# Optimization experiments

Measured on AMD Instinct MI355X. Metric: run time of the kernel, lower is better.

The kernel has to match this reference:

```python
import jax, jax.numpy as jnp
import numpy as np

N, E, HDIM, EDIM, MSG_H, UPD_H = 50000, 640000, 128, 32, 128, 128
LN_EPS = 1e-5


def setup_inputs() -> dict:
    key = jax.random.key(0)
    ks = jax.random.split(key, 12)
    def lin(k, fan_in, fan_out):
        return jax.random.normal(k, (fan_in, fan_out), dtype=jnp.float32) / np.sqrt(fan_in)
    h = jax.random.normal(ks[0], (N, HDIM), dtype=jnp.float32)
    edge_index = jax.random.randint(ks[1], (2, E), 0, N, dtype=jnp.int32)
    edge_attr = jax.random.normal(ks[2], (E, EDIM), dtype=jnp.float32)
    return {
        "h": h,
        "edge_index": edge_index,
        "edge_attr": edge_attr,
        # edge MLP: Linear(2*hdim+edim -> msg_hidden), ReLU, Linear(msg_hidden -> hdim)
        "ew1": lin(ks[3], 2 * HDIM + EDIM, MSG_H),
        "eb1": jnp.zeros((MSG_H,), jnp.float32),
        "ew2": lin(ks[4], MSG_H, HDIM),
        "eb2": jnp.zeros((HDIM,), jnp.float32),
        # node MLP: Linear(2*hdim -> upd_hidden), ReLU, Linear(upd_hidden -> hdim)
        "nw1": lin(ks[5], 2 * HDIM, UPD_H),
        "nb1": jnp.zeros((UPD_H,), jnp.float32),
        "nw2": lin(ks[6], UPD_H, HDIM),
        "nb2": jnp.zeros((HDIM,), jnp.float32),
        # LayerNorm(hdim)
        "gamma": jnp.ones((HDIM,), jnp.float32),
        "beta": jnp.zeros((HDIM,), jnp.float32),
    }


def reference(h, edge_index, edge_attr, ew1, eb1, ew2, eb2, nw1, nb1, nw2, nb2, gamma, beta):
    src, dst = edge_index[0], edge_index[1]
    # gather + concat -> edge MLP  (eval mode: dropout inactive, edge_dropout off)
    m_in = jnp.concatenate([h[src], h[dst], edge_attr], axis=1)       # [E, 2H+EDIM]
    m = jax.nn.relu(m_in @ ew1 + eb1) @ ew2 + eb2                     # [E, H]
    # scatter-add messages into destination nodes
    agg = jax.ops.segment_sum(m, dst, num_segments=h.shape[0])        # [N, H]
    # node update MLP
    u_in = jnp.concatenate([h, agg], axis=1)                          # [N, 2H]
    h_upd = jax.nn.relu(u_in @ nw1 + nb1) @ nw2 + nb2                 # [N, H]
    # residual + LayerNorm
    x = h + h_upd
    mu = jnp.mean(x, axis=-1, keepdims=True)
    var = jnp.mean(jnp.square(x - mu), axis=-1, keepdims=True)
    return (x - mu) * jax.lax.rsqrt(var + LN_EPS) * gamma + beta
```

## Files before the change

### kernel.cpp

```cpp
#include <hip/hip_runtime.h>
#include <cstdint>

#define HD 128
#define ED 32
#define BME 64
#define BMN 128
#define PAD_E 296
#define PAD_N 264
#define PAD_T 136
#define EGRID 512

typedef _Float16 f16;
typedef __attribute__((ext_vector_type(2))) _Float16 f16x2;
typedef __attribute__((ext_vector_type(4))) _Float16 f16x4;
typedef __attribute__((ext_vector_type(8))) _Float16 f16x8;
typedef __attribute__((ext_vector_type(4))) float    f32x4;

__device__ __forceinline__ f32x4 mfma16(f16x8 a, f16x8 b, f32x4 c) {
    return __builtin_amdgcn_mfma_f32_16x16x32_f16(a, b, c, 0, 0, 0);
}
__device__ __forceinline__ f16x8 cvt8(const float* p) {
    const float4 a0 = *(const float4*)p;
    const float4 a1 = *(const float4*)(p + 4);
    f16x8 v;
    v[0] = (f16)a0.x; v[1] = (f16)a0.y; v[2] = (f16)a0.z; v[3] = (f16)a0.w;
    v[4] = (f16)a1.x; v[5] = (f16)a1.y; v[6] = (f16)a1.z; v[7] = (f16)a1.w;
    return v;
}

__global__ __launch_bounds__(256) void zero_f32(float4* p, long n4) {
    long i = (long)blockIdx.x * blockDim.x + threadIdx.x;
    const long stride = (long)gridDim.x * blockDim.x;
    const float4 z = make_float4(0.f, 0.f, 0.f, 0.f);
    for (; i < n4; i += stride) p[i] = z;
}
__global__ __launch_bounds__(256) void zero_i32(int* p, int n) {
    int i = blockIdx.x * blockDim.x + threadIdx.x;
    if (i < n) p[i] = 0;
}
__global__ __launch_bounds__(256)
void cvt_f16_kernel(const float* __restrict__ x, f16* __restrict__ y, long n8) {
    long i = blockIdx.x * 256 + threadIdx.x;
    const long stride = (long)gridDim.x * 256;
    for (; i < n8; i += stride) *(f16x8*)(y + i * 8) = cvt8(x + i * 8);
}
__global__ __launch_bounds__(256)
void pack_all_kernel(const float* __restrict__ ew1, const float* __restrict__ ew2,
                     const float* __restrict__ nw1, const float* __restrict__ nw2,
                     f16* __restrict__ w1p, f16* __restrict__ w2p,
                     f16* __restrict__ n1p, f16* __restrict__ n2p)
{
    const int b = blockIdx.x;
    const float* w; f16* wp; int base;
    if (b < 18)      { w = ew1; wp = w1p; base = b; }
    else if (b < 26) { w = ew2; wp = w2p; base = b - 18; }
    else if (b < 42) { w = nw1; wp = n1p; base = b - 26; }
    else             { w = nw2; wp = n2p; base = b - 42; }
    const int idx = base * 256 + threadIdx.x;
    const int l  = idx & 63;
    const int fr = idx >> 6;
    const int ht = fr & 1, wvv = (fr >> 1) & 3, kt = fr >> 3;
    const int lii = l & 15, qq = l >> 4;
    const float* p = w + (size_t)(32 * kt + 8 * qq) * HD + 32 * wvv + 16 * ht + lii;
    f16x8 v;
#pragma unroll
    for (int e2 = 0; e2 < 8; ++e2) v[e2] = (f16)p[(size_t)e2 * HD];
    *(f16x8*)(wp + (size_t)idx * 8) = v;
}

__global__ __launch_bounds__(256)
void hist_kernel(const int* __restrict__ eidx, int* __restrict__ rank,
                 int* __restrict__ cnt, int E) {
    int e = blockIdx.x * 256 + threadIdx.x;
    if (e < E) rank[e] = atomicAdd(&cnt[eidx[E + e]], 1);
}
__global__ __launch_bounds__(1024)
void scan_kernel(const int* __restrict__ cnt, int* __restrict__ rs, int N) {
    __shared__ int wsum[16];
    __shared__ int s_carry;
    const int t = threadIdx.x, lane = t & 63, wid = t >> 6;
    if (t == 0) s_carry = 0;
    __syncthreads();
    for (int base = 0; base < N; base += 1024) {
        const int i = base + t;
        const int v = (i < N) ? cnt[i] : 0;
        int incl = v;
#pragma unroll
        for (int off = 1; off < 64; off <<= 1) {
            int u = __shfl_up(incl, off, 64);
            if (lane >= off) incl += u;
        }
        if (lane == 63) wsum[wid] = incl;
        __syncthreads();
        if (t == 0) {
            int s = 0;
#pragma unroll
            for (int w = 0; w < 16; ++w) { int x = wsum[w]; wsum[w] = s; s += x; }
        }
        __syncthreads();
        const int carry = s_carry;
        if (i < N) rs[i] = carry + wsum[wid] + incl - v;
        __syncthreads();
        if (t == 1023) s_carry = carry + wsum[15] + incl;
        __syncthreads();
    }
    if (threadIdx.x == 0) rs[N] = s_carry;
}
__global__ __launch_bounds__(256)
void pos_kernel(const int* __restrict__ eidx, const int* __restrict__ rs,
                int* __restrict__ pos, int E) {
    int e = blockIdx.x * 256 + threadIdx.x;
    if (e < E) pos[e] = rs[eidx[E + e]] + pos[e];
}

template <int MODE>
__global__ __launch_bounds__(256, 2)
void edge_kernel(const f16*   __restrict__ h16,
                 const int*   __restrict__ eidx,
                 const float* __restrict__ ea,
                 const f16*   __restrict__ w1p,
                 const float* __restrict__ b1,
                 const f16*   __restrict__ w2p,
                 const float* __restrict__ b2,
                 void*        __restrict__ aggm,
                 const int*   __restrict__ pos,
                 int E, int ntiles)
{
    __shared__ __align__(16) f16 sA[BME * PAD_E];
    __shared__ __align__(16) f16 sT[BME * PAD_T];
    __shared__ int sIdx[2][BME];

    const int t  = threadIdx.x;
    const int l  = t & 63;
    const int wv = t >> 6;
    const int li = l & 15;
    const int q  = l >> 4;
    const int r  = t >> 2;
    const int q4 = t & 3;

    f16x8 A1[2][9], A2[2][4];
#pragma unroll
    for (int ht = 0; ht < 2; ++ht) {
#pragma unroll
        for (int kt = 0; kt < 9; ++kt)
            A1[ht][kt] = *(const f16x8*)(w1p + ((size_t)(kt * 8 + wv * 2 + ht) * 64 + l) * 8);
#pragma unroll
        for (int kt = 0; kt < 4; ++kt)
            A2[ht][kt] = *(const f16x8*)(w2p + ((size_t)(kt * 8 + wv * 2 + ht) * 64 + l) * 8);
    }

    f16x8 d[9];
    int   psr = 0;
    auto prefetch = [&](int tile) {
        const int ec  = min(tile * BME + r, E - 1);
        const int src = eidx[ec];
        const int dst = eidx[E + ec];
        psr = (MODE == 0) ? dst : pos[ec];
        const f16* hs = h16 + (size_t)src * HD;
        const f16* hd = h16 + (size_t)dst * HD;
        const float* eap = ea + (size_t)ec * ED;
#pragma unroll
        for (int i = 0; i < 9; ++i) {
            const int c = q4 * 72 + i * 8;
            d[i] = (c < HD)     ? *(const f16x8*)(hs + c)
                 : (c < 2 * HD) ? *(const f16x8*)(hd + c - HD)
                                : cvt8(eap + (c - 2 * HD));
        }
    };

    int tb = blockIdx.x;
    if (tb < ntiles) prefetch(tb);
    int par = 0;

    for (; tb < ntiles; tb += gridDim.x, par ^= 1) {
#pragma unroll
        for (int i = 0; i < 9; ++i)
            *(f16x8*)(sA + r * PAD_E + q4 * 72 + i * 8) = d[i];
        if (q4 == 0) sIdx[par][r] = psr;
        __syncthreads();

        const int nt = tb + gridDim.x;
        if (nt < ntiles) prefetch(nt);

        f32x4 acc[2][4];
#pragma unroll
        for (int i = 0; i < 2; ++i)
#pragma unroll
            for (int j = 0; j < 4; ++j) acc[i][j] = (f32x4){0.f, 0.f, 0.f, 0.f};
#pragma unroll
        for (int kt = 0; kt < 9; ++kt) {
#pragma unroll
            for (int et = 0; et < 4; ++et) {
                const f16x8 b = *(const f16x8*)(sA + (16 * et + li) * PAD_E + 32 * kt + 8 * q);
                acc[0][et] = mfma16(A1[0][kt], b, acc[0][et]);
                acc[1][et] = mfma16(A1[1][kt], b, acc[1][et]);
            }
        }

#pragma unroll
        for (int ht = 0; ht < 2; ++ht) {
            const int hidb = 32 * wv + 16 * ht + 4 * q;
            const float4 bb = *(const float4*)(b1 + hidb);
#pragma unroll
            for (int et = 0; et < 4; ++et) {
                const f32x4 v = acc[ht][et];
                float x0 = v[0] + bb.x, x1 = v[1] + bb.y,
                      x2 = v[2] + bb.z, x3 = v[3] + bb.w;
                x0 = x0 > 0.f ? x0 : 0.f;  x1 = x1 > 0.f ? x1 : 0.f;
                x2 = x2 > 0.f ? x2 : 0.f;  x3 = x3 > 0.f ? x3 : 0.f;
                f16x4 o; o[0] = (f16)x0; o[1] = (f16)x1; o[2] = (f16)x2; o[3] = (f16)x3;
                *(f16x4*)(sT + (16 * et + li) * PAD_T + hidb) = o;
            }
        }
        __syncthreads();

        f32x4 acc2[2][4];
#pragma unroll
        for (int i = 0; i < 2; ++i)
#pragma unroll
            for (int j = 0; j < 4; ++j) acc2[i][j] = (f32x4){0.f, 0.f, 0.f, 0.f};
#pragma unroll
        for (int kt = 0; kt < 4; ++kt) {
#pragma unroll
            for (int et = 0; et < 4; ++et) {
                const f16x8 b = *(const f16x8*)(sT + (16 * et + li) * PAD_T + 32 * kt + 8 * q);
                acc2[0][et] = mfma16(A2[0][kt], b, acc2[0][et]);
                acc2[1][et] = mfma16(A2[1][kt], b, acc2[1][et]);
            }
        }

        if (MODE == 0) {
            float* agg = (float*)aggm;
#pragma unroll
            for (int ht = 0; ht < 2; ++ht) {
                const int hidb = 32 * wv + 16 * ht + 4 * q;
                const float4 bb = *(const float4*)(b2 + hidb);
#pragma unroll
                for (int et = 0; et < 4; ++et) {
                    const int edge = 16 * et + li;
                    if (tb * BME + edge < E) {
                        float* p = agg + (size_t)sIdx[par][edge] * HD + hidb;
                        const f32x4 v = acc2[ht][et];
                        atomicAdd(p + 0, v[0] + bb.x);
                        atomicAdd(p + 1, v[1] + bb.y);
                        atomicAdd(p + 2, v[2] + bb.z);
                        atomicAdd(p + 3, v[3] + bb.w);
                    }
                }
            }
            __syncthreads();
        } else {
            __syncthreads();
#pragma unroll
            for (int ht = 0; ht < 2; ++ht) {
                const int hidb = 32 * wv + 16 * ht + 4 * q;
                const float4 bb = *(const float4*)(b2 + hidb);
#pragma unroll
                for (int et = 0; et < 4; ++et) {
                    const f32x4 v = acc2[ht][et];
                    f16x4 o;
                    o[0] = (f16)(v[0] + bb.x); o[1] = (f16)(v[1] + bb.y);
                    o[2] = (f16)(v[2] + bb.z); o[3] = (f16)(v[3] + bb.w);
                    *(f16x4*)(sT + (16 * et + li) * PAD_T + hidb) = o;
                }
            }
            __syncthreads();
            f16* m = (f16*)aggm;
#pragma unroll
            for (int i = 0; i < 4; ++i) {
                const int idx = t + i * 256;
                const int row = idx >> 4;
                const int c8  = (idx & 15) * 8;
                if (tb * BME + row < E) {
                    const f16x8 v = *(const f16x8*)(sT + row * PAD_T + c8);
                    *(f16x8*)(m + (size_t)sIdx[par][row] * HD + c8) = v;
                }
            }
        }
    }
}

__global__ __launch_bounds__(256)
void gather_kernel(const f16* __restrict__ m, const int* __restrict__ rs,
                   f16* __restrict__ aggb, int N)
{
    const int n = blockIdx.x * 4 + (threadIdx.x >> 6);
    if (n >= N) return;
    const int lane = threadIdx.x & 63;
    const int s = rs[n], e = rs[n + 1];
    const f16* base = m + (size_t)s * HD + lane * 2;
    const int cnt = e - s;
    float a0 = 0.f, b0 = 0.f, a1 = 0.f, b1 = 0.f;
    int j = 0;
    for (; j + 2 <= cnt; j += 2) {
        const f16x2 u = *(const f16x2*)(base + (size_t)j * HD);
        const f16x2 v = *(const f16x2*)(base + (size_t)(j + 1) * HD);
        a0 += (float)u[0]; b0 += (float)u[1];
        a1 += (float)v[0]; b1 += (float)v[1];
    }
    if (j < cnt) {
        const f16x2 u = *(const f16x2*)(base + (size_t)j * HD);
        a0 += (float)u[0]; b0 += (float)u[1];
    }
    f16x2 rr; rr[0] = (f16)(a0 + a1); rr[1] = (f16)(b0 + b1);
    *(f16x2*)(aggb + (size_t)n * HD + lane * 2) = rr;
}

template <int CSR>
__global__ __launch_bounds__(256, 2)
void node_kernel(const f16*   __restrict__ h16,
                 const float* __restrict__ h,
                 const f16*   __restrict__ aggb,
                 const float* __restrict__ aggf,
                 const f16*   __restrict__ w1p,
                 const float* __restrict__ b1,
                 const f16*   __restrict__ w2p,
                 const float* __restrict__ b2,
                 const float* __restrict__ gamma,
                 const float* __restrict__ beta,
                 float*       __restrict__ out,
                 int N)
{
    __shared__ __align__(16) f16 sA[BMN * PAD_N];
    __shared__ float sMV[2 * BMN];

    const int t  = threadIdx.x;
    const int l  = t & 63;
    const int wv = t >> 6;
    const int li = l & 15;
    const int q  = l >> 4;
    const int nbase = blockIdx.x * BMN;

    {
        const int r = t >> 1, half = t & 1;
        const int node = min(nbase + r, N - 1);
        f16* rowp = sA + r * PAD_N + half * HD;
        if (half == 0) {
            const f16* src = h16 + (size_t)node * HD;
#pragma unroll
            for (int i = 0; i < 16; ++i)
                *(f16x8*)(rowp + i * 8) = *(const f16x8*)(src + i * 8);
        } else if (CSR) {
            const f16* src = aggb + (size_t)node * HD;
#pragma unroll
            for (int i = 0; i < 16; ++i)
                *(f16x8*)(rowp + i * 8) = *(const f16x8*)(src + i * 8);
        } else {
            const float* src = aggf + (size_t)node * HD;
#pragma unroll
            for (int i = 0; i < 16; ++i)
                *(f16x8*)(rowp + i * 8) = cvt8(src + i * 8);
        }
    }

    f16x8 A1[2][8];
#pragma unroll
    for (int ht = 0; ht < 2; ++ht)
#pragma unroll
        for (int kt = 0; kt < 8; ++kt)
            A1[ht][kt] = *(const f16x8*)(w1p + ((size_t)(kt * 8 + wv * 2 + ht) * 64 + l) * 8);
    __syncthreads();

    f32x4 acc[2][8];
#pragma unroll
    for (int i = 0; i < 2; ++i)
#pragma unroll
        for (int j = 0; j < 8; ++j) acc[i][j] = (f32x4){0.f, 0.f, 0.f, 0.f};
#pragma unroll
    for (int kt = 0; kt < 8; ++kt) {
#pragma unroll
        for (int et = 0; et < 8; ++et) {
            const f16x8 b = *(const f16x8*)(sA + (16 * et + li) * PAD_N + 32 * kt + 8 * q);
            acc[0][et] = mfma16(A1[0][kt], b, acc[0][et]);
            acc[1][et] = mfma16(A1[1][kt], b, acc[1][et]);
        }
    }
    __syncthreads();

    f16x8 A2[2][4];
#pragma unroll
    for (int ht = 0; ht < 2; ++ht)
#pragma unroll
        for (int kt = 0; kt < 4; ++kt)
            A2[ht][kt] = *(const f16x8*)(w2p + ((size_t)(kt * 8 + wv * 2 + ht) * 64 + l) * 8);

    f16* sT = sA;
#pragma unroll
    for (int ht = 0; ht < 2; ++ht) {
        const int hidb = 32 * wv + 16 * ht + 4 * q;
        const float4 bb = *(const float4*)(b1 + hidb);
#pragma unroll
        for (int et = 0; et < 8; ++et) {
            const f32x4 v = acc[ht][et];
            float x0 = v[0] + bb.x, x1 = v[1] + bb.y,
                  x2 = v[2] + bb.z, x3 = v[3] + bb.w;
            x0 = x0 > 0.f ? x0 : 0.f;  x1 = x1 > 0.f ? x1 : 0.f;
            x2 = x2 > 0.f ? x2 : 0.f;  x3 = x3 > 0.f ? x3 : 0.f;
            f16x4 o; o[0] = (f16)x0; o[1] = (f16)x1; o[2] = (f16)x2; o[3] = (f16)x3;
            *(f16x4*)(sT + (16 * et + li) * PAD_T + hidb) = o;
        }
    }
    __syncthreads();

    f32x4 acc2[2][8];
#pragma unroll
    for (int i = 0; i < 2; ++i)
#pragma unroll
        for (int j = 0; j < 8; ++j) acc2[i][j] = (f32x4){0.f, 0.f, 0.f, 0.f};
#pragma unroll
    for (int kt = 0; kt < 4; ++kt) {
#pragma unroll
        for (int et = 0; et < 8; ++et) {
            const f16x8 b = *(const f16x8*)(sT + (16 * et + li) * PAD_T + 32 * kt + 8 * q);
            acc2[0][et] = mfma16(A2[0][kt], b, acc2[0][et]);
            acc2[1][et] = mfma16(A2[1][kt], b, acc2[1][et]);
        }
    }
    __syncthreads();

    float* sX = (float*)sA;
#pragma unroll
    for (int ht = 0; ht < 2; ++ht) {
        const int hidb = 32 * wv + 16 * ht + 4 * q;
        const float4 bb = *(const float4*)(b2 + hidb);
#pragma unroll
        for (int et = 0; et < 8; ++et) {
            const int node = 16 * et + li;
            const int nc   = min(nbase + node, N - 1);
            const float4 hv = *(const float4*)(h + (size_t)nc * HD + hidb);
            const f32x4 v = acc2[ht][et];
            f32x4 x;
            x[0] = v[0] + bb.x + hv.x;
            x[1] = v[1] + bb.y + hv.y;
            x[2] = v[2] + bb.z + hv.z;
            x[3] = v[3] + bb.w + hv.w;
            *(f32x4*)(sX + (size_t)node * 132 + hidb) = x;
        }
    }
    __syncthreads();

    {
        const int node  = t >> 1;
        const int half2 = t & 1;
        const float* px = sX + node * 132 + half2 * 64;
        float s = 0.f, sq = 0.f;
#pragma unroll
        for (int i = 0; i < 16; ++i) {
            const float4 v = *(const float4*)(px + i * 4);
            s  += v.x + v.y + v.z + v.w;
            sq += v.x * v.x + v.y * v.y + v.z * v.z + v.w * v.w;
        }
        s  += __shfl_xor(s, 1);
        sq += __shfl_xor(sq, 1);
        if (!half2) {
            const float mean = s * (1.f / HD);
            const float var  = sq * (1.f / HD) - mean * mean;
            sMV[node]       = mean;
            sMV[BMN + node] = rsqrtf(var + 1e-5f);
        }
    }
    __syncthreads();

#pragma unroll
    for (int i = 0; i < 16; ++i) {
        const int idx  = t + i * 256;
        const int node = idx >> 5;
        const int c4   = (idx & 31) * 4;
        if (nbase + node < N) {
            const float4 xv = *(const float4*)(sX + node * 132 + c4);
            const float4 g4 = *(const float4*)(gamma + c4);
            const float4 b4 = *(const float4*)(beta + c4);
            const float mean = sMV[node];
            const float rstd = sMV[BMN + node];
            float4 o;
            o.x = (xv.x - mean) * rstd * g4.x + b4.x;
            o.y = (xv.y - mean) * rstd * g4.y + b4.y;
            o.z = (xv.z - mean) * rstd * g4.z + b4.z;
            o.w = (xv.w - mean) * rstd * g4.w + b4.w;
            *(float4*)(out + (size_t)(nbase + node) * HD + c4) = o;
        }
    }
}

extern "C" void kernel_launch(void* const* d_in, const int* in_sizes, int n_in,
                              void* d_out, int out_size, void* d_ws, size_t ws_size,
                              hipStream_t stream)
{
    const float* h     = (const float*)d_in[0];
    const int*   eidx  = (const int*)  d_in[1];
    const float* ea    = (const float*)d_in[2];
    const float* ew1   = (const float*)d_in[3];
    const float* eb1   = (const float*)d_in[4];
    const float* ew2   = (const float*)d_in[5];
    const float* eb2   = (const float*)d_in[6];
    const float* nw1   = (const float*)d_in[7];
    const float* nb1   = (const float*)d_in[8];
    const float* nw2   = (const float*)d_in[9];
    const float* nb2   = (const float*)d_in[10];
    const float* gamma = (const float*)d_in[11];
    const float* beta  = (const float*)d_in[12];
    float* out = (float*)d_out;

    const int N = in_sizes[0] / HD;
    const int E = in_sizes[1] / 2;
    const int ntiles = (E + BME - 1) / BME;

    size_t off = 0;
    auto alloc = [&](size_t bytes) {
        size_t o = off; off += (bytes + 255) & ~(size_t)255; return o;
    };
    const size_t o_m    = alloc((size_t)E * HD * sizeof(f16));
    const size_t o_agb  = alloc((size_t)N * HD * sizeof(f16));
    const size_t o_h16  = alloc((size_t)N * HD * sizeof(f16));
    const size_t o_pos  = alloc((size_t)E * sizeof(int));
    const size_t o_rs   = alloc((size_t)(N + 1) * sizeof(int));
    const size_t o_cnt  = alloc((size_t)N * sizeof(int));
    const size_t o_w1p  = alloc((size_t)9 * 8 * 64 * 8 * sizeof(f16));
    const size_t o_w2p  = alloc((size_t)4 * 8 * 64 * 8 * sizeof(f16));
    const size_t o_n1p  = alloc((size_t)8 * 8 * 64 * 8 * sizeof(f16));
    const size_t o_n2p  = alloc((size_t)4 * 8 * 64 * 8 * sizeof(f16));
    const bool csr = (off <= ws_size);
    char* ws = (char*)d_ws;

    if (csr) {
        f16* mb   = (f16*)(ws + o_m);
        f16* aggb = (f16*)(ws + o_agb);
        f16* h16  = (f16*)(ws + o_h16);
        int* pos  = (int*)(ws + o_pos);
        int* rs   = (int*)(ws + o_rs);
        int* cnt  = (int*)(ws + o_cnt);
        f16* w1p  = (f16*)(ws + o_w1p);
        f16* w2p  = (f16*)(ws + o_w2p);
        f16* n1p  = (f16*)(ws + o_n1p);
        f16* n2p  = (f16*)(ws + o_n2p);

        zero_i32<<<(N + 255) / 256, 256, 0, stream>>>(cnt, N);
        hist_kernel<<<(E + 255) / 256, 256, 0, stream>>>(eidx, pos, cnt, E);
        scan_kernel<<<1, 1024, 0, stream>>>(cnt, rs, N);
        pos_kernel<<<(E + 255) / 256, 256, 0, stream>>>(eidx, rs, pos, E);
        cvt_f16_kernel<<<2048, 256, 0, stream>>>(h, h16, (long)N * HD / 8);
        pack_all_kernel<<<50, 256, 0, stream>>>(ew1, ew2, nw1, nw2, w1p, w2p, n1p, n2p);
        edge_kernel<1><<<EGRID, 256, 0, stream>>>(
            h16, eidx, ea, w1p, eb1, w2p, eb2, (void*)mb, pos, E, ntiles);
        gather_kernel<<<(N + 3) / 4, 256, 0, stream>>>(mb, rs, aggb, N);
        node_kernel<1><<<(N + BMN - 1) / BMN, 256, 0, stream>>>(
            h16, h, aggb, nullptr, n1p, nb1, n2p, nb2, gamma, beta, out, N);
    } else {
        size_t foff = 0;
        auto falloc = [&](size_t bytes) {
            size_t o = foff; foff += (bytes + 255) & ~(size_t)255; return o;
        };
        float* agg = (float*)(ws + falloc((size_t)N * HD * sizeof(float)));
        f16*   h16 = (f16*)  (ws + falloc((size_t)N * HD * sizeof(f16)));
        f16*   w1p = (f16*)  (ws + falloc((size_t)9 * 8 * 64 * 8 * sizeof(f16)));
        f16*   w2p = (f16*)  (ws + falloc((size_t)4 * 8 * 64 * 8 * sizeof(f16)));
        f16*   n1p = (f16*)  (ws + falloc((size_t)8 * 8 * 64 * 8 * sizeof(f16)));
        f16*   n2p = (f16*)  (ws + falloc((size_t)4 * 8 * 64 * 8 * sizeof(f16)));

        zero_f32<<<1024, 256, 0, stream>>>((float4*)agg, (long)N * HD / 4);
        cvt_f16_kernel<<<2048, 256, 0, stream>>>(h, h16, (long)N * HD / 8);
        pack_all_kernel<<<50, 256, 0, stream>>>(ew1, ew2, nw1, nw2, w1p, w2p, n1p, n2p);
        edge_kernel<0><<<EGRID, 256, 0, stream>>>(
            h16, eidx, ea, w1p, eb1, w2p, eb2, (void*)agg, nullptr, E, ntiles);
        node_kernel<0><<<(N + BMN - 1) / BMN, 256, 0, stream>>>(
            h16, h, nullptr, agg, n1p, nb1, n2p, nb2, gamma, beta, out, N);
    }
}
```

Measured before the change: 298.0 us.

## Use 8-wave edge blocks with XOR-swizzled LDS and nontemporal message traffic

Doubles the edge-kernel block to 512 threads so each wave owns 16 hidden columns instead of 32, halving per-wave weight registers and accumulators to raise occupancy. LDS tiles are now unpadded, and 16-byte chunks are XOR-swizzled by row to avoid bank conflicts, with the weight packing relaid to match. Message writes and gather reads use nontemporal hints to keep the streaming message buffer from polluting cache. The trade-off is more waves sharing each B-fragment load, plus extra swizzle index arithmetic.

```diff
diff --git a/kernel.cpp b/kernel.cpp
--- a/kernel.cpp
+++ b/kernel.cpp
@@ -5,7 +5,6 @@
 #define ED 32
 #define BME 64
 #define BMN 128
-#define PAD_E 296
 #define PAD_N 264
 #define PAD_T 136
 #define EGRID 512
@@ -15,6 +14,7 @@
 typedef __attribute__((ext_vector_type(4))) _Float16 f16x4;
 typedef __attribute__((ext_vector_type(8))) _Float16 f16x8;
 typedef __attribute__((ext_vector_type(4))) float    f32x4;
+typedef __attribute__((ext_vector_type(4))) unsigned int u32x4;
 
 __device__ __forceinline__ f32x4 mfma16(f16x8 a, f16x8 b, f32x4 c) {
     return __builtin_amdgcn_mfma_f32_16x16x32_f16(a, b, c, 0, 0, 0);
@@ -59,9 +59,9 @@
     const int idx = base * 256 + threadIdx.x;
     const int l  = idx & 63;
     const int fr = idx >> 6;
-    const int ht = fr & 1, wvv = (fr >> 1) & 3, kt = fr >> 3;
+    const int wi = fr & 7, kt = fr >> 3;
     const int lii = l & 15, qq = l >> 4;
-    const float* p = w + (size_t)(32 * kt + 8 * qq) * HD + 32 * wvv + 16 * ht + lii;
+    const float* p = w + (size_t)(32 * kt + 8 * qq) * HD + 16 * wi + lii;
     f16x8 v;
 #pragma unroll
     for (int e2 = 0; e2 < 8; ++e2) v[e2] = (f16)p[(size_t)e2 * HD];
@@ -114,7 +114,7 @@
 }
 
 template <int MODE>
-__global__ __launch_bounds__(256, 2)
+__global__ __launch_bounds__(512, 4)
 void edge_kernel(const f16*   __restrict__ h16,
                  const int*   __restrict__ eidx,
                  const float* __restrict__ ea,
@@ -126,8 +126,8 @@
                  const int*   __restrict__ pos,
                  int E, int ntiles)
 {
-    __shared__ __align__(16) f16 sA[BME * PAD_E];
-    __shared__ __align__(16) f16 sT[BME * PAD_T];
+    __shared__ __align__(16) f16 sA[BME * 320];
+    __shared__ __align__(16) f16 sT[BME * 128];
     __shared__ int sIdx[2][BME];
 
     const int t  = threadIdx.x;
@@ -135,21 +135,20 @@
     const int wv = t >> 6;
     const int li = l & 15;
     const int q  = l >> 4;
-    const int r  = t >> 2;
-    const int q4 = t & 3;
-
-    f16x8 A1[2][9], A2[2][4];
-#pragma unroll
-    for (int ht = 0; ht < 2; ++ht) {
-#pragma unroll
-        for (int kt = 0; kt < 9; ++kt)
-            A1[ht][kt] = *(const f16x8*)(w1p + ((size_t)(kt * 8 + wv * 2 + ht) * 64 + l) * 8);
-#pragma unroll
-        for (int kt = 0; kt < 4; ++kt)
-            A2[ht][kt] = *(const f16x8*)(w2p + ((size_t)(kt * 8 + wv * 2 + ht) * 64 + l) * 8);
-    }
-
-    f16x8 d[9];
+    const int lm = l & 7;
+    const int r  = t >> 3;
+    const int q8 = t & 7;
+
+    f16x8 A1[9], A2[4];
+#pragma unroll
+    for (int kt = 0; kt < 9; ++kt)
+        A1[kt] = *(const f16x8*)(w1p + ((size_t)(kt * 8 + wv) * 64 + l) * 8);
+#pragma unroll
+    for (int kt = 0; kt < 4; ++kt)
+        A2[kt] = *(const f16x8*)(w2p + ((size_t)(kt * 8 + wv) * 64 + l) * 8);
+
+    f16x8 d[4];
+    f16x8 d4;
     int   psr = 0;
     auto prefetch = [&](int tile) {
         const int ec  = min(tile * BME + r, E - 1);
@@ -158,14 +157,13 @@
         psr = (MODE == 0) ? dst : pos[ec];
         const f16* hs = h16 + (size_t)src * HD;
         const f16* hd = h16 + (size_t)dst * HD;
-        const float* eap = ea + (size_t)ec * ED;
-#pragma unroll
-        for (int i = 0; i < 9; ++i) {
-            const int c = q4 * 72 + i * 8;
-            d[i] = (c < HD)     ? *(const f16x8*)(hs + c)
-                 : (c < 2 * HD) ? *(const f16x8*)(hd + c - HD)
-                                : cvt8(eap + (c - 2 * HD));
-        }
+#pragma unroll
+        for (int i = 0; i < 4; ++i) {
+            const int c = (q8 + 8 * i) * 8;
+            d[i] = (c < HD) ? *(const f16x8*)(hs + c)
+                            : *(const f16x8*)(hd + (c - HD));
+        }
+        if (q8 < 4) d4 = cvt8(ea + (size_t)ec * ED + q8 * 8);
     };
 
     int tb = blockIdx.x;
@@ -173,107 +171,110 @@
     int par = 0;
 
     for (; tb < ntiles; tb += gridDim.x, par ^= 1) {
-#pragma unroll
-        for (int i = 0; i < 9; ++i)
-            *(f16x8*)(sA + r * PAD_E + q4 * 72 + i * 8) = d[i];
-        if (q4 == 0) sIdx[par][r] = psr;
+        {
+            f16* row = sA + r * 320;
+            const int sw = r & 7;
+#pragma unroll
+            for (int i = 0; i < 4; ++i) {
+                const int ch = q8 + 8 * i;
+                *(f16x8*)(row + ((ch ^ sw) * 8)) = d[i];
+            }
+            if (q8 < 4)
+                *(f16x8*)(row + (((q8 + 32) ^ sw) * 8)) = d4;
+            if (q8 == 0) sIdx[par][r] = psr;
+        }
         __syncthreads();
 
-        const int nt = tb + gridDim.x;
+        const int nt = tb + (int)gridDim.x;
         if (nt < ntiles) prefetch(nt);
 
-        f32x4 acc[2][4];
-#pragma unroll
-        for (int i = 0; i < 2; ++i)
-#pragma unroll
-            for (int j = 0; j < 4; ++j) acc[i][j] = (f32x4){0.f, 0.f, 0.f, 0.f};
+        f32x4 acc[4];
+#pragma unroll
+        for (int j = 0; j < 4; ++j) acc[j] = (f32x4){0.f, 0.f, 0.f, 0.f};
 #pragma unroll
         for (int kt = 0; kt < 9; ++kt) {
 #pragma unroll
             for (int et = 0; et < 4; ++et) {
-                const f16x8 b = *(const f16x8*)(sA + (16 * et + li) * PAD_E + 32 * kt + 8 * q);
-                acc[0][et] = mfma16(A1[0][kt], b, acc[0][et]);
-                acc[1][et] = mfma16(A1[1][kt], b, acc[1][et]);
-            }
-        }
-
-#pragma unroll
-        for (int ht = 0; ht < 2; ++ht) {
-            const int hidb = 32 * wv + 16 * ht + 4 * q;
+                const f16x8 b = *(const f16x8*)(sA + (16 * et + li) * 320
+                                                + (((4 * kt + q) ^ lm) * 8));
+                acc[et] = mfma16(A1[kt], b, acc[et]);
+            }
+        }
+
+        {
+            const int hidb = 16 * wv + 4 * q;
             const float4 bb = *(const float4*)(b1 + hidb);
+            const int chT = hidb >> 3;
+            const int off = hidb & 7;
 #pragma unroll
             for (int et = 0; et < 4; ++et) {
-                const f32x4 v = acc[ht][et];
-                float x0 = v[0] + bb.x, x1 = v[1] + bb.y,
-                      x2 = v[2] + bb.z, x3 = v[3] + bb.w;
-                x0 = x0 > 0.f ? x0 : 0.f;  x1 = x1 > 0.f ? x1 : 0.f;
-                x2 = x2 > 0.f ? x2 : 0.f;  x3 = x3 > 0.f ? x3 : 0.f;
+                const f32x4 v = acc[et];
+                float x0 = fmaxf(v[0] + bb.x, 0.f), x1 = fmaxf(v[1] + bb.y, 0.f);
+                float x2 = fmaxf(v[2] + bb.z, 0.f), x3 = fmaxf(v[3] + bb.w, 0.f);
                 f16x4 o; o[0] = (f16)x0; o[1] = (f16)x1; o[2] = (f16)x2; o[3] = (f16)x3;
-                *(f16x4*)(sT + (16 * et + li) * PAD_T + hidb) = o;
+                *(f16x4*)(sT + (16 * et + li) * 128 + ((chT ^ lm) * 8) + off) = o;
             }
         }
         __syncthreads();
 
-        f32x4 acc2[2][4];
-#pragma unroll
-        for (int i = 0; i < 2; ++i)
-#pragma unroll
-            for (int j = 0; j < 4; ++j) acc2[i][j] = (f32x4){0.f, 0.f, 0.f, 0.f};
+        f32x4 acc2[4];
+#pragma unroll
+        for (int j = 0; j < 4; ++j) acc2[j] = (f32x4){0.f, 0.f, 0.f, 0.f};
 #pragma unroll
         for (int kt = 0; kt < 4; ++kt) {
 #pragma unroll
             for (int et = 0; et < 4; ++et) {
-                const f16x8 b = *(const f16x8*)(sT + (16 * et + li) * PAD_T + 32 * kt + 8 * q);
-                acc2[0][et] = mfma16(A2[0][kt], b, acc2[0][et]);
-                acc2[1][et] = mfma16(A2[1][kt], b, acc2[1][et]);
+                const f16x8 b = *(const f16x8*)(sT + (16 * et + li) * 128
+                                                + (((4 * kt + q) ^ lm) * 8));
+                acc2[et] = mfma16(A2[kt], b, acc2[et]);
             }
         }
 
         if (MODE == 0) {
             float* agg = (float*)aggm;
-#pragma unroll
-            for (int ht = 0; ht < 2; ++ht) {
-                const int hidb = 32 * wv + 16 * ht + 4 * q;
-                const float4 bb = *(const float4*)(b2 + hidb);
-#pragma unroll
-                for (int et = 0; et < 4; ++et) {
-                    const int edge = 16 * et + li;
-                    if (tb * BME + edge < E) {
-                        float* p = agg + (size_t)sIdx[par][edge] * HD + hidb;
-                        const f32x4 v = acc2[ht][et];
-                        atomicAdd(p + 0, v[0] + bb.x);
-                        atomicAdd(p + 1, v[1] + bb.y);
-                        atomicAdd(p + 2, v[2] + bb.z);
-                        atomicAdd(p + 3, v[3] + bb.w);
-                    }
+            const int hidb = 16 * wv + 4 * q;
+            const float4 bb = *(const float4*)(b2 + hidb);
+#pragma unroll
+            for (int et = 0; et < 4; ++et) {
+                const int edge = 16 * et + li;
+                if (tb * BME + edge < E) {
+                    float* p = agg + (size_t)sIdx[par][edge] * HD + hidb;
+                    const f32x4 v = acc2[et];
+                    atomicAdd(p + 0, v[0] + bb.x);
+                    atomicAdd(p + 1, v[1] + bb.y);
+                    atomicAdd(p + 2, v[2] + bb.z);
+                    atomicAdd(p + 3, v[3] + bb.w);
                 }
             }
             __syncthreads();
         } else {
             __syncthreads();
-#pragma unroll
-            for (int ht = 0; ht < 2; ++ht) {
-                const int hidb = 32 * wv + 16 * ht + 4 * q;
+            {
+                const int hidb = 16 * wv + 4 * q;
                 const float4 bb = *(const float4*)(b2 + hidb);
+                const int chT = hidb >> 3;
+                const int off = hidb & 7;
 #pragma unroll
                 for (int et = 0; et < 4; ++et) {
-                    const f32x4 v = acc2[ht][et];
+                    const f32x4 v = acc2[et];
                     f16x4 o;
                     o[0] = (f16)(v[0] + bb.x); o[1] = (f16)(v[1] + bb.y);
                     o[2] = (f16)(v[2] + bb.z); o[3] = (f16)(v[3] + bb.w);
-                    *(f16x4*)(sT + (16 * et + li) * PAD_T + hidb) = o;
+                    *(f16x4*)(sT + (16 * et + li) * 128 + ((chT ^ lm) * 8) + off) = o;
                 }
             }
             __syncthreads();
             f16* m = (f16*)aggm;
 #pragma unroll
-            for (int i = 0; i < 4; ++i) {
-                const int idx = t + i * 256;
-                const int row = idx >> 4;
-                const int c8  = (idx & 15) * 8;
-                if (tb * BME + row < E) {
-                    const f16x8 v = *(const f16x8*)(sT + row * PAD_T + c8);
-                    *(f16x8*)(m + (size_t)sIdx[par][row] * HD + c8) = v;
+            for (int i = 0; i < 2; ++i) {
+                const int idx  = t + i * 512;
+                const int row2 = idx >> 4;
+                const int c    = idx & 15;
+                if (tb * BME + row2 < E) {
+                    const f16x8 v = *(const f16x8*)(sT + row2 * 128
+                                                    + ((c ^ (row2 & 7)) * 8));
+                    __builtin_nontemporal_store(*(const u32x4*)&v,
+                        (u32x4*)(m + (size_t)sIdx[par][row2] * HD + c * 8));
                 }
             }
         }
@@ -293,13 +294,19 @@
     float a0 = 0.f, b0 = 0.f, a1 = 0.f, b1 = 0.f;
     int j = 0;
     for (; j + 2 <= cnt; j += 2) {
-        const f16x2 u = *(const f16x2*)(base + (size_t)j * HD);
-        const f16x2 v = *(const f16x2*)(base + (size_t)(j + 1) * HD);
+        const unsigned int uu = __builtin_nontemporal_load(
+            (const unsigned int*)(base + (size_t)j * HD));
+        const unsigned int vv = __builtin_nontemporal_load(
+            (const unsigned int*)(base + (size_t)(j + 1) * HD));
+        const f16x2 u = *(const f16x2*)&uu;
+        const f16x2 v = *(const f16x2*)&vv;
         a0 += (float)u[0]; b0 += (float)u[1];
         a1 += (float)v[0]; b1 += (float)v[1];
     }
     if (j < cnt) {
-        const f16x2 u = *(const f16x2*)(base + (size_t)j * HD);
+        const unsigned int uu = __builtin_nontemporal_load(
+            (const unsigned int*)(base + (size_t)j * HD));
+        const f16x2 u = *(const f16x2*)&uu;
         a0 += (float)u[0]; b0 += (float)u[1];
     }
     f16x2 rr; rr[0] = (f16)(a0 + a1); rr[1] = (f16)(b0 + b1);
@@ -392,10 +399,8 @@
 #pragma unroll
         for (int et = 0; et < 8; ++et) {
             const f32x4 v = acc[ht][et];
-            float x0 = v[0] + bb.x, x1 = v[1] + bb.y,
-                  x2 = v[2] + bb.z, x3 = v[3] + bb.w;
-            x0 = x0 > 0.f ? x0 : 0.f;  x1 = x1 > 0.f ? x1 : 0.f;
-            x2 = x2 > 0.f ? x2 : 0.f;  x3 = x3 > 0.f ? x3 : 0.f;
+            float x0 = fmaxf(v[0] + bb.x, 0.f), x1 = fmaxf(v[1] + bb.y, 0.f);
+            float x2 = fmaxf(v[2] + bb.z, 0.f), x3 = fmaxf(v[3] + bb.w, 0.f);
             f16x4 o; o[0] = (f16)x0; o[1] = (f16)x1; o[2] = (f16)x2; o[3] = (f16)x3;
             *(f16x4*)(sT + (16 * et + li) * PAD_T + hidb) = o;
         }
@@ -540,7 +545,7 @@
         pos_kernel<<<(E + 255) / 256, 256, 0, stream>>>(eidx, rs, pos, E);
         cvt_f16_kernel<<<2048, 256, 0, stream>>>(h, h16, (long)N * HD / 8);
         pack_all_kernel<<<50, 256, 0, stream>>>(ew1, ew2, nw1, nw2, w1p, w2p, n1p, n2p);
-        edge_kernel<1><<<EGRID, 256, 0, stream>>>(
+        edge_kernel<1><<<EGRID, 512, 0, stream>>>(
             h16, eidx, ea, w1p, eb1, w2p, eb2, (void*)mb, pos, E, ntiles);
         gather_kernel<<<(N + 3) / 4, 256, 0, stream>>>(mb, rs, aggb, N);
         node_kernel<1><<<(N + BMN - 1) / BMN, 256, 0, stream>>>(
@@ -560,7 +565,7 @@
         zero_f32<<<1024, 256, 0, stream>>>((float4*)agg, (long)N * HD / 4);
         cvt_f16_kernel<<<2048, 256, 0, stream>>>(h, h16, (long)N * HD / 8);
         pack_all_kernel<<<50, 256, 0, stream>>>(ew1, ew2, nw1, nw2, w1p, w2p, n1p, n2p);
-        edge_kernel<0><<<EGRID, 256, 0, stream>>>(
+        edge_kernel<0><<<EGRID, 512, 0, stream>>>(
             h16, eidx, ea, w1p, eb1, w2p, eb2, (void*)agg, nullptr, E, ntiles);
         node_kernel<0><<<(N + BMN - 1) / BMN, 256, 0, stream>>>(
             h16, h, nullptr, agg, n1p, nb1, n2p, nb2, gamma, beta, out, N);
```

Result: faster. 281.7 us (-5.5%).
